# Performance work log

Measured on AMD Instinct MI355X. Metric: run time of the kernel, lower is better.

## Reference

```python
import jax, jax.numpy as jnp
import numpy as np
import math

B, S, D = 2, 2048, 1024
H, KV, HD = 16, 4, 64
G = H // KV          # kv groups
CAP = 50.0           # attention soft-cap
EPS = 1e-6           # RMSNorm eps


def _rmsnorm(x, w):
    return x * jax.lax.rsqrt(jnp.mean(x * x, axis=-1, keepdims=True) + EPS) * w


def _rope(x, freqs):
    # x: (b, h, s, hd); freqs: (S, hd//2, 2) with [...,0]=cos, [...,1]=sin
    s = x.shape[2]
    xp = x.reshape(*x.shape[:-1], -1, 2)
    cos = freqs[:s, :, 0][None, None]   # (1,1,s,hd//2)
    sin = freqs[:s, :, 1][None, None]
    x0, x1 = xp[..., 0], xp[..., 1]
    out = jnp.stack([x0 * cos - x1 * sin, x0 * sin + x1 * cos], axis=-1)
    return out.reshape(x.shape)


def setup_inputs() -> dict:
    key = jax.random.key(0)
    ks = jax.random.split(key, 6)
    x = jax.random.normal(ks[0], (B, S, D), dtype=jnp.float32)
    # realistic RoPE table: theta_i = pos / 10000^(2i/hd)
    inv_freq = 1.0 / (10000.0 ** (np.arange(0, HD, 2, dtype=np.float32) / HD))
    theta = np.arange(S, dtype=np.float32)[:, None] * inv_freq[None, :]
    rope_freqs = jnp.asarray(np.stack([np.cos(theta), np.sin(theta)], axis=-1))
    sc = 0.02
    wq = jax.random.normal(ks[1], (2 * H * HD, D), dtype=jnp.float32) * sc
    wk = jax.random.normal(ks[2], (2 * KV * HD, D), dtype=jnp.float32) * sc
    wv = jax.random.normal(ks[3], (KV * HD, D), dtype=jnp.float32) * sc
    wo = jax.random.normal(ks[4], (D, H * HD), dtype=jnp.float32) * sc
    q_norm_w = jnp.ones((HD,), dtype=jnp.float32)
    k_norm_w = jnp.ones((HD,), dtype=jnp.float32)
    diff_lambda = jnp.array([0.8], dtype=jnp.float32)
    return {"x": x, "rope_freqs": rope_freqs, "wq": wq, "wk": wk, "wv": wv,
            "wo": wo, "q_norm_w": q_norm_w, "k_norm_w": k_norm_w,
            "diff_lambda": diff_lambda}


def reference(x, rope_freqs, wq, wk, wv, wo, q_norm_w, k_norm_w, diff_lambda):
    b, s, _ = x.shape
    # projections (torch Linear: y = x @ W^T)
    q = (x @ wq.T).reshape(b, s, H, 2 * HD).transpose(0, 2, 1, 3)   # (b,H,s,2hd)
    k = (x @ wk.T).reshape(b, s, KV, 2 * HD).transpose(0, 2, 1, 3)  # (b,KV,s,2hd)
    v = (x @ wv.T).reshape(b, s, KV, HD).transpose(0, 2, 1, 3)      # (b,KV,s,hd)
    q1, q2 = jnp.split(q, 2, axis=-1)
    k1, k2 = jnp.split(k, 2, axis=-1)
    # QK-norm (before RoPE, as in the torch module)
    q1, q2 = _rmsnorm(q1, q_norm_w), _rmsnorm(q2, q_norm_w)
    k1, k2 = _rmsnorm(k1, k_norm_w), _rmsnorm(k2, k_norm_w)
    # RoPE
    q1, q2 = _rope(q1, rope_freqs), _rope(q2, rope_freqs)
    k1, k2 = _rope(k1, rope_freqs), _rope(k2, rope_freqs)
    # GQA expansion: each kv head repeated G times contiguously
    k1 = jnp.repeat(k1, G, axis=1)
    k2 = jnp.repeat(k2, G, axis=1)
    v = jnp.repeat(v, G, axis=1)
    scale = 1.0 / math.sqrt(HD)
    scores1 = jnp.einsum('bhqd,bhkd->bhqk', q1, k1) * scale
    scores2 = jnp.einsum('bhqd,bhkd->bhqk', q2, k2) * scale
    # soft-cap
    scores1 = CAP * jnp.tanh(scores1 / CAP)
    scores2 = CAP * jnp.tanh(scores2 / CAP)
    mask = jnp.triu(jnp.full((s, s), -jnp.inf, dtype=scores1.dtype), 1)
    attn1 = jax.nn.softmax(scores1 + mask, axis=-1)
    attn2 = jax.nn.softmax(scores2 + mask, axis=-1)
    diff_attn = attn1 - diff_lambda[0] * attn2
    out = jnp.einsum('bhqk,bhkd->bhqd', diff_attn, v)
    out = out.transpose(0, 2, 1, 3).reshape(b, s, H * HD)
    return out @ wo.T
```

## Files before the change

kernel.cpp:

```cpp
#include <hip/hip_runtime.h>
#include <hip/hip_bf16.h>

#define B_ 2
#define S_ 2048
#define D_ 1024
#define H_ 16
#define KV_ 4
#define HD_ 64
#define G_ (H_ / KV_)
#define NCAT 2816
#define VOFF 2560

typedef __attribute__((ext_vector_type(8))) short short8;
typedef __attribute__((ext_vector_type(4))) short short4v;
typedef __attribute__((ext_vector_type(2))) int int2v;
typedef __attribute__((ext_vector_type(4))) int int4v;
typedef __attribute__((ext_vector_type(4))) float floatx4;

using gvoid_p = const __attribute__((address_space(1))) void*;
using lvoid_p = __attribute__((address_space(3))) void*;

__device__ inline void gload_lds16(const short* g, short* l) {
    __builtin_amdgcn_global_load_lds((gvoid_p)(const void*)g, (lvoid_p)(void*)l, 16, 0, 0);
}

__device__ inline int cvt_pk_bf16(float lo, float hi) {
    int r;
    asm volatile("v_cvt_pk_bf16_f32 %0, %1, %2" : "=v"(r) : "v"(lo), "v"(hi));
    return r;
}

__global__ void cvt5_kernel(const float* s0, const float* s1, const float* s2,
                            const float* s3, const float* s4,
                            __hip_bfloat16* d0, __hip_bfloat16* d1, __hip_bfloat16* d2,
                            __hip_bfloat16* d3, __hip_bfloat16* d4,
                            int n0, int n1, int n2, int n3, int n4) {
    const float* s; __hip_bfloat16* d; int n;
    switch (blockIdx.y) {
        case 0: s = s0; d = d0; n = n0; break;
        case 1: s = s1; d = d1; n = n1; break;
        case 2: s = s2; d = d2; n = n2; break;
        case 3: s = s3; d = d3; n = n3; break;
        default: s = s4; d = d4; n = n4; break;
    }
    int nv = n >> 2;
    for (int i = blockIdx.x * blockDim.x + threadIdx.x; i < nv;
         i += gridDim.x * blockDim.x) {
        floatx4 v = ((const floatx4*)s)[i];
        short4v o;
#pragma unroll
        for (int e = 0; e < 4; ++e) {
            __hip_bfloat16 hh = __float2bfloat16(v[e]);
            o[e] = __builtin_bit_cast(short, hh);
        }
        ((short4v*)d)[i] = o;
    }
}

template <typename OutT>
__global__ __launch_bounds__(256) void gemm_bt_lds(const short* __restrict__ A,
                                                   const short* __restrict__ Bm,
                                                   OutT* __restrict__ C,
                                                   int M, int N, int K) {
    __shared__ __align__(16) short As[2][128 * 32];
    __shared__ __align__(16) short Bs[2][128 * 32];
    int tid = threadIdx.x;
    int wid = tid >> 6, lane = tid & 63;
    int wr = wid >> 1, wc = wid & 1;
    int r = lane & 15, kq = lane >> 4;

    int nwg = gridDim.x * gridDim.y;
    int orig = blockIdx.y * gridDim.x + blockIdx.x;
    int wg = (orig & 7) * (nwg >> 3) + (orig >> 3);
    int bx = wg % gridDim.x, by = wg / gridDim.x;

    long m0 = (long)by * 128;
    long n0 = (long)bx * 128;

    const short* gA0 = A + (m0 + (tid >> 2)) * (long)K + (tid & 3) * 8;
    const short* gA1 = A + (m0 + 64 + (tid >> 2)) * (long)K + (tid & 3) * 8;
    const short* gB0 = Bm + (n0 + (tid >> 2)) * (long)K + (tid & 3) * 8;
    const short* gB1 = Bm + (n0 + 64 + (tid >> 2)) * (long)K + (tid & 3) * 8;

    auto stage = [&](int buf, int k0) {
        gload_lds16(gA0 + k0, &As[buf][wid * 512]);
        gload_lds16(gA1 + k0, &As[buf][2048 + wid * 512]);
        gload_lds16(gB0 + k0, &Bs[buf][wid * 512]);
        gload_lds16(gB1 + k0, &Bs[buf][2048 + wid * 512]);
    };

    floatx4 acc[4][4];
#pragma unroll
    for (int i = 0; i < 4; ++i)
#pragma unroll
        for (int j = 0; j < 4; ++j) acc[i][j] = {0.f, 0.f, 0.f, 0.f};

    int nt = K >> 5;
    stage(0, 0);
    for (int t = 0; t < nt; ++t) {
        int cur = t & 1;
        __builtin_amdgcn_s_barrier();
        if (t + 1 < nt) {
            stage(cur ^ 1, (t + 1) << 5);
            asm volatile("s_waitcnt vmcnt(4)" ::: "memory");
        } else {
            asm volatile("s_waitcnt vmcnt(0)" ::: "memory");
        }
        __builtin_amdgcn_sched_barrier(0);
        __builtin_amdgcn_s_barrier();
        short8 a[4], b[4];
#pragma unroll
        for (int mi = 0; mi < 4; ++mi)
            a[mi] = *(const short8*)&As[cur][(wr * 64 + mi * 16 + r) * 32 + kq * 8];
#pragma unroll
        for (int ni = 0; ni < 4; ++ni)
            b[ni] = *(const short8*)&Bs[cur][(wc * 64 + ni * 16 + r) * 32 + kq * 8];
#pragma unroll
        for (int mi = 0; mi < 4; ++mi)
#pragma unroll
            for (int ni = 0; ni < 4; ++ni)
                acc[mi][ni] = __builtin_amdgcn_mfma_f32_16x16x32_bf16(
                    a[mi], b[ni], acc[mi][ni], 0, 0, 0);
    }
    int col_l = lane & 15, row_l = (lane >> 4) * 4;
#pragma unroll
    for (int mi = 0; mi < 4; ++mi)
#pragma unroll
        for (int ni = 0; ni < 4; ++ni) {
            long col = n0 + wc * 64 + ni * 16 + col_l;
            long row0 = m0 + wr * 64 + mi * 16 + row_l;
#pragma unroll
            for (int j = 0; j < 4; ++j) {
                float v = acc[mi][ni][j];
                if constexpr (__is_same(OutT, float))
                    C[(row0 + j) * N + col] = v;
                else
                    C[(row0 + j) * N + col] = __float2bfloat16(v);
            }
        }
}

__global__ void norm_rope_kernel(const __hip_bfloat16* __restrict__ buf,
                                 __hip_bfloat16* __restrict__ outb,
                                 const float* __restrict__ freqs,
                                 const float* __restrict__ w, int nvec, int nh,
                                 int tstride, int colbase) {
    int gt = blockIdx.x * blockDim.x + threadIdx.x;
    int gw = gt >> 6;
    int lane = gt & 63;
    if (gw >= nvec) return;
    int t = gw / (nh * 2);
    int rem = gw - t * (nh * 2);
    int s = t & (S_ - 1);
    const __hip_bfloat16* v = buf + (long)t * tstride + colbase + rem * 64;
    float x = __bfloat162float(v[lane]);
    float ss = x * x;
#pragma unroll
    for (int off = 32; off; off >>= 1) ss += __shfl_xor(ss, off);
    float r = rsqrtf(ss * (1.f / 64.f) + 1e-6f);
    x = x * r * w[lane];
    int i = lane >> 1;
    float c  = freqs[(s * (HD_ / 2) + i) * 2];
    float sn = freqs[(s * (HD_ / 2) + i) * 2 + 1];
    float p = __shfl_xor(x, 1);
    float y = (lane & 1) ? fmaf(p, sn, x * c) : fmaf(x, c, -(p * sn));
    outb[(long)gw * 64 + lane] = __float2bfloat16(y);
}

__global__ __launch_bounds__(256) void v_transpose_kernel(const short* __restrict__ src,
                                                          short* __restrict__ dst) {
    __shared__ short ls[64][72];
    int s0 = blockIdx.x * 64;
    int kv = blockIdx.y, b = blockIdx.z;
    int tid = threadIdx.x;
    const short* base = src + ((long)(b * S_ + s0)) * NCAT + VOFF + kv * 64;
    {
        int rr = tid >> 2, cc = (tid & 3) * 16;
        *(short8*)&ls[rr][cc]     = *(const short8*)(base + (long)rr * NCAT + cc);
        *(short8*)&ls[rr][cc + 8] = *(const short8*)(base + (long)rr * NCAT + cc + 8);
    }
    __syncthreads();
    short* ob = dst + ((long)(b * KV_ + kv) * 64) * S_ + s0;
    {
        int d = tid >> 2, sl = (tid & 3) * 16;
        short8 o0, o1;
#pragma unroll
        for (int e = 0; e < 8; ++e) { o0[e] = ls[sl + e][d]; o1[e] = ls[sl + 8 + e][d]; }
        *(short8*)(ob + (long)d * S_ + sl)     = o0;
        *(short8*)(ob + (long)d * S_ + sl + 8) = o1;
    }
}

__global__ __launch_bounds__(256, 4) void attn_kernel(const short* __restrict__ qb,
                                                      const short* __restrict__ kbuf,
                                                      const short* __restrict__ vtb,
                                                      __hip_bfloat16* __restrict__ ob,
                                                      float* __restrict__ part,
                                                      float* __restrict__ lpart,
                                                      const float* __restrict__ lam_p) {
    __shared__ __align__(16) short Ks[3][32][128];
    __shared__ __align__(16) short Vt[2][64][40];

    int tid = threadIdx.x, w = tid >> 6, lane = tid & 63;
    int b = blockIdx.z, h = blockIdx.y, kv = h / G_;
    int p = (int)blockIdx.x >> 1, e = (int)blockIdx.x & 1;
    int qtA = p, qtB = 31 - p;
    int r = lane & 15, kq = lane >> 4;
    float lam = lam_p[0];

    floatx4 acc[2][4];
    floatx4 accl[2];
    short8 qa[2][2];

    const short* vbase = vtb + (long)(b * KV_ + kv) * 64 * S_;
    const float c1 = 0.18033688f, nc4 = -3.7570e-7f, zoff = -17.3123405f;
    const short one_bf = (short)0x3F80;
    short8 ones8 = {one_bf, one_bf, one_bf, one_bf, one_bf, one_bf, one_bf, one_bf};

    int ch1 = tid + 256;
    int krow0 = tid >> 4, kcs0 = ((tid & 15) ^ (krow0 & 7)) * 8;
    int krow1 = ch1 >> 4, kcs1 = ((ch1 & 15) ^ (krow1 & 7)) * 8;
    const short* kgb = kbuf + ((long)b * S_ * KV_ + kv) * 128;
    int vd = tid >> 2, vch = tid & 3;

    auto issueK = [&](int buf, int ki) {
        long rb = (long)(ki * 32) * (KV_ * 128);
        gload_lds16(kgb + rb + (long)krow0 * (KV_ * 128) + kcs0, &Ks[buf][0][0] + w * 512);
        gload_lds16(kgb + rb + (long)krow1 * (KV_ * 128) + kcs1, &Ks[buf][0][0] + 2048 + w * 512);
    };
    auto loadV = [&](int kb) {
        return *(const short8*)(vbase + (long)vd * S_ + kb + vch * 8);
    };

    auto reset_acc = [&]() {
#pragma unroll
        for (int m = 0; m < 2; ++m) {
            accl[m] = {0.f, 0.f, 0.f, 0.f};
#pragma unroll
            for (int dt = 0; dt < 4; ++dt) acc[m][dt] = {0.f, 0.f, 0.f, 0.f};
        }
    };
    auto load_q = [&](int q0) {
        const short* qrow = qb + ((long)(b * S_ + q0 + r) * H_ + h) * 128;
        qa[0][0] = *(const short8*)(qrow + kq * 8);
        qa[0][1] = *(const short8*)(qrow + 32 + kq * 8);
        qa[1][0] = *(const short8*)(qrow + 64 + kq * 8);
        qa[1][1] = *(const short8*)(qrow + 96 + kq * 8);
    };

    auto tile_compute = [&](int bk, int cv, int kb, int q0, bool domask) {
        int rel = q0 + r - kb;
        short8 vb[4];
#pragma unroll
        for (int dt = 0; dt < 4; ++dt) {
            const short* vrow = &Vt[cv][dt * 16 + r][0];
            int2v lo = *(const int2v*)(vrow + 4 * kq);
            int2v hi = *(const int2v*)(vrow + 16 + 4 * kq);
            vb[dt] = __builtin_bit_cast(short8, int4v{lo[0], lo[1], hi[0], hi[1]});
        }
#pragma unroll
        for (int m = 0; m < 2; ++m) {
            floatx4 sacc[2];
#pragma unroll
            for (int nt = 0; nt < 2; ++nt) {
                sacc[nt] = {0.f, 0.f, 0.f, 0.f};
                const short* row = &Ks[bk][nt * 16 + r][0];
                short8 a0 = *(const short8*)(row + (((m * 8) + kq) ^ (r & 7)) * 8);
                short8 a1 = *(const short8*)(row + (((m * 8) + 4 + kq) ^ (r & 7)) * 8);
                sacc[nt] = __builtin_amdgcn_mfma_f32_16x16x32_bf16(a0, qa[m][0], sacc[nt], 0, 0, 0);
                sacc[nt] = __builtin_amdgcn_mfma_f32_16x16x32_bf16(a1, qa[m][1], sacc[nt], 0, 0, 0);
            }
            float pv[2][4];
#pragma unroll
            for (int nt = 0; nt < 2; ++nt)
#pragma unroll
                for (int j = 0; j < 4; ++j) {
                    float raw = sacc[nt][j];
                    float r2 = raw * raw;
                    float z = fmaf(raw, fmaf(r2, nc4, c1), zoff);
                    pv[nt][j] = __builtin_amdgcn_exp2f(z);
                }
            if (domask) {
#pragma unroll
                for (int nt = 0; nt < 2; ++nt)
#pragma unroll
                    for (int j = 0; j < 4; ++j)
                        if (nt * 16 + kq * 4 + j > rel) pv[nt][j] = 0.f;
            }
            int d0 = cvt_pk_bf16(pv[0][0], pv[0][1]);
            int d1 = cvt_pk_bf16(pv[0][2], pv[0][3]);
            int d2 = cvt_pk_bf16(pv[1][0], pv[1][1]);
            int d3 = cvt_pk_bf16(pv[1][2], pv[1][3]);
            short8 pa8 = __builtin_bit_cast(short8, int4v{d0, d1, d2, d3});
#pragma unroll
            for (int dt = 0; dt < 4; ++dt)
                acc[m][dt] = __builtin_amdgcn_mfma_f32_16x16x32_bf16(
                    pa8, vb[dt], acc[m][dt], 0, 0, 0);
            accl[m] = __builtin_amdgcn_mfma_f32_16x16x32_bf16(pa8, ones8, accl[m], 0, 0, 0);
        }
    };

    auto run = [&](int qt, int ki0, int ki1, bool diag) {
        int q0 = qt * 64 + w * 16;
        load_q(q0);
        reset_acc();
        int nseg = ki1 - ki0;
        issueK(0, ki0);
        short8 rva = loadV(ki0 * 32), rvb;
        int bk = 0;
        for (int ii = 0; ii < nseg; ++ii) {
            int ki = ki0 + ii, cv = ii & 1;
            bool pre = (ii + 1 < nseg);
            int bk1 = (bk == 2) ? 0 : bk + 1;
            if (pre) issueK(bk1, ki + 1);
            if (pre) asm volatile("s_waitcnt vmcnt(2)" ::: "memory");
            else     asm volatile("s_waitcnt vmcnt(0)" ::: "memory");
            __builtin_amdgcn_sched_barrier(0);
            if (cv == 0) {
                *(short8*)&Vt[0][vd][vch * 8] = rva;
                if (pre) rvb = loadV((ki + 1) * 32);
            } else {
                *(short8*)&Vt[1][vd][vch * 8] = rvb;
                if (pre) rva = loadV((ki + 1) * 32);
            }
            asm volatile("s_waitcnt lgkmcnt(0)" ::: "memory");
            __builtin_amdgcn_sched_barrier(0);
            __builtin_amdgcn_s_barrier();
            tile_compute(bk, cv, ki * 32, q0, diag && ((ki >> 1) == qt));
            bk = bk1;
        }
        __builtin_amdgcn_s_barrier();
    };

    if (e == 0) {
        run(qtA, 0, 2 * qtA + 2, true);
        {
            int q0 = qtA * 64 + w * 16;
#pragma unroll
            for (int j = 0; j < 4; ++j) {
                float i1 = 1.f / accl[0][j];
                float i2 = lam / accl[1][j];
                int qr = q0 + kq * 4 + j;
                __hip_bfloat16* orow = ob + ((long)(b * S_ + qr) * H_ + h) * 64;
#pragma unroll
                for (int dt = 0; dt < 4; ++dt) {
                    float val = acc[0][dt][j] * i1 - acc[1][dt][j] * i2;
                    orow[dt * 16 + r] = __float2bfloat16(val);
                }
            }
        }
        run(qtB, 0, 31 - 2 * p, false);
    } else {
        run(qtB, 31 - 2 * p, 64 - 2 * p, true);
    }

    {
        long slot = (long)(b * H_ + h) * 16 + (qtB - 16);
        long base = ((slot * 2 + e) * 2) * 4096L;
        int qloc = w * 16 + kq * 4;
#pragma unroll
        for (int m = 0; m < 2; ++m)
#pragma unroll
            for (int dt = 0; dt < 4; ++dt)
#pragma unroll
                for (int j = 0; j < 4; ++j)
                    part[base + m * 4096L + (qloc + j) * 64 + dt * 16 + r] = acc[m][dt][j];
        if (r == 0) {
#pragma unroll
            for (int m = 0; m < 2; ++m)
#pragma unroll
                for (int j = 0; j < 4; ++j)
                    lpart[((slot * 2 + e) * 2 + m) * 64 + qloc + j] = accl[m][j];
        }
    }
}

__global__ __launch_bounds__(256) void attn_merge_kernel(const float* __restrict__ part,
                                                         const float* __restrict__ lpart,
                                                         __hip_bfloat16* __restrict__ ob,
                                                         const float* __restrict__ lam_p) {
    long sid = blockIdx.x;
    int t16 = sid & 15;
    int h = (sid >> 4) & (H_ - 1);
    int b = (int)(sid >> 8);
    int qt = 16 + t16;
    float lam = lam_p[0];
    const float* p0 = part + sid * 4 * 4096L;
    const float* p1 = part + (sid * 4 + 2) * 4096L;
    const float* l0 = lpart + sid * 4 * 64L;
    const float* l1 = lpart + (sid * 4 + 2) * 64L;
    int tid = threadIdx.x;
#pragma unroll
    for (int i = 0; i < 16; ++i) {
        int idx = i * 256 + tid;
        int q = idx >> 6, d = idx & 63;
        float a1 = p0[q * 64 + d] + p1[q * 64 + d];
        float a2 = p0[4096 + q * 64 + d] + p1[4096 + q * 64 + d];
        float L1 = l0[q] + l1[q];
        float L2 = l0[64 + q] + l1[64 + q];
        float val = a1 / L1 - lam * (a2 / L2);
        ob[((long)(b * S_ + qt * 64 + q) * H_ + h) * 64 + d] = __float2bfloat16(val);
    }
}

extern "C" void kernel_launch(void* const* d_in, const int* in_sizes, int n_in,
                              void* d_out, int out_size, void* d_ws, size_t ws_size,
                              hipStream_t stream) {
    const float* x     = (const float*)d_in[0];
    const float* freqs = (const float*)d_in[1];
    const float* wq    = (const float*)d_in[2];
    const float* wk    = (const float*)d_in[3];
    const float* wv    = (const float*)d_in[4];
    const float* wo    = (const float*)d_in[5];
    const float* qnw   = (const float*)d_in[6];
    const float* knw   = (const float*)d_in[7];
    const float* lam   = (const float*)d_in[8];
    float* out = (float*)d_out;

    const int T = B_ * S_;
    char* ws = (char*)d_ws;
    size_t off = 0;
    auto alloc = [&](size_t bytes) {
        void* p = ws + off;
        off += (bytes + 255) & ~(size_t)255;
        return p;
    };
    __hip_bfloat16* xb   = (__hip_bfloat16*)alloc((size_t)T * D_ * 2);
    __hip_bfloat16* wcat = (__hip_bfloat16*)alloc((size_t)NCAT * D_ * 2);
    __hip_bfloat16* wob  = (__hip_bfloat16*)alloc((size_t)D_ * D_ * 2);
    __hip_bfloat16* qkvb = (__hip_bfloat16*)alloc((size_t)T * NCAT * 2);
    __hip_bfloat16* qb16 = (__hip_bfloat16*)alloc((size_t)T * 2 * H_ * HD_ * 2);
    __hip_bfloat16* kb16 = (__hip_bfloat16*)alloc((size_t)T * 2 * KV_ * HD_ * 2);
    __hip_bfloat16* vT   = (__hip_bfloat16*)alloc((size_t)B_ * KV_ * HD_ * S_ * 2);
    float* part  = (float*)alloc((size_t)512 * 2 * 2 * 4096 * 4);
    float* lpart = (float*)alloc((size_t)512 * 2 * 2 * 64 * 4);
    __hip_bfloat16* aob  = xb;

    cvt5_kernel<<<dim3(2048, 5), 256, 0, stream>>>(
        x, wq, wk, wv, wo,
        xb, wcat, wcat + (size_t)2 * H_ * HD_ * D_,
        wcat + (size_t)(2 * H_ * HD_ + 2 * KV_ * HD_) * D_, wob,
        T * D_, 2 * H_ * HD_ * D_, 2 * KV_ * HD_ * D_, KV_ * HD_ * D_, D_ * D_);

    gemm_bt_lds<__hip_bfloat16><<<dim3(NCAT / 128, T / 128), 256, 0, stream>>>(
        (const short*)xb, (const short*)wcat, qkvb, T, NCAT, D_);

    {
        int nvq = T * H_ * 2;
        norm_rope_kernel<<<(nvq * 64 + 255) / 256, 256, 0, stream>>>(
            qkvb, qb16, freqs, qnw, nvq, H_, NCAT, 0);
        int nvk = T * KV_ * 2;
        norm_rope_kernel<<<(nvk * 64 + 255) / 256, 256, 0, stream>>>(
            qkvb, kb16, freqs, knw, nvk, KV_, NCAT, 2 * H_ * HD_);
        v_transpose_kernel<<<dim3(S_ / 64, KV_, B_), 256, 0, stream>>>(
            (const short*)qkvb, (short*)vT);
    }

    attn_kernel<<<dim3(32, H_, B_), 256, 0, stream>>>(
        (const short*)qb16, (const short*)kb16, (const short*)vT, aob, part, lpart, lam);
    attn_merge_kernel<<<512, 256, 0, stream>>>(part, lpart, aob, lam);

    gemm_bt_lds<float><<<dim3(D_ / 128, T / 128), 256, 0, stream>>>(
        (const short*)aob, (const short*)wob, out, T, D_, D_);
}
```

Before: 174.6 us.

## Remap attention grid per XCD, add MFMA priority hints, pack partials to bf16

```diff
diff --git a/kernel.cpp b/kernel.cpp
--- a/kernel.cpp
+++ b/kernel.cpp
@@ -28,6 +28,13 @@
     int r;
     asm volatile("v_cvt_pk_bf16_f32 %0, %1, %2" : "=v"(r) : "v"(lo), "v"(hi));
     return r;
+}
+
+__device__ inline float bf16lo(unsigned u) {
+    return __builtin_bit_cast(float, u << 16);
+}
+__device__ inline float bf16hi(unsigned u) {
+    return __builtin_bit_cast(float, u & 0xffff0000u);
 }
 
 __global__ void cvt5_kernel(const float* s0, const float* s1, const float* s2,
@@ -195,15 +202,20 @@
                                                       const short* __restrict__ kbuf,
                                                       const short* __restrict__ vtb,
                                                       __hip_bfloat16* __restrict__ ob,
-                                                      float* __restrict__ part,
+                                                      unsigned* __restrict__ part,
                                                       float* __restrict__ lpart,
                                                       const float* __restrict__ lam_p) {
     __shared__ __align__(16) short Ks[3][32][128];
     __shared__ __align__(16) short Vt[2][64][40];
 
     int tid = threadIdx.x, w = tid >> 6, lane = tid & 63;
-    int b = blockIdx.z, h = blockIdx.y, kv = h / G_;
-    int p = (int)blockIdx.x >> 1, e = (int)blockIdx.x & 1;
+    int raw = (int)blockIdx.x;
+    int xcd = raw & 7;
+    int kv = xcd & 3, b = xcd >> 2;
+    int i5 = raw >> 3;
+    int x = i5 & 31, hh = i5 >> 5;
+    int h = kv * G_ + hh;
+    int p = x >> 1, e = x & 1;
     int qtA = p, qtB = 31 - p;
     int r = lane & 15, kq = lane >> 4;
     float lam = lam_p[0];
@@ -261,6 +273,7 @@
 #pragma unroll
         for (int m = 0; m < 2; ++m) {
             floatx4 sacc[2];
+            __builtin_amdgcn_s_setprio(1);
 #pragma unroll
             for (int nt = 0; nt < 2; ++nt) {
                 sacc[nt] = {0.f, 0.f, 0.f, 0.f};
@@ -270,14 +283,15 @@
                 sacc[nt] = __builtin_amdgcn_mfma_f32_16x16x32_bf16(a0, qa[m][0], sacc[nt], 0, 0, 0);
                 sacc[nt] = __builtin_amdgcn_mfma_f32_16x16x32_bf16(a1, qa[m][1], sacc[nt], 0, 0, 0);
             }
+            __builtin_amdgcn_s_setprio(0);
             float pv[2][4];
 #pragma unroll
             for (int nt = 0; nt < 2; ++nt)
 #pragma unroll
                 for (int j = 0; j < 4; ++j) {
-                    float raw = sacc[nt][j];
-                    float r2 = raw * raw;
-                    float z = fmaf(raw, fmaf(r2, nc4, c1), zoff);
+                    float rawv = sacc[nt][j];
+                    float r2 = rawv * rawv;
+                    float z = fmaf(rawv, fmaf(r2, nc4, c1), zoff);
                     pv[nt][j] = __builtin_amdgcn_exp2f(z);
                 }
             if (domask) {
@@ -292,11 +306,13 @@
             int d2 = cvt_pk_bf16(pv[1][0], pv[1][1]);
             int d3 = cvt_pk_bf16(pv[1][2], pv[1][3]);
             short8 pa8 = __builtin_bit_cast(short8, int4v{d0, d1, d2, d3});
+            __builtin_amdgcn_s_setprio(1);
 #pragma unroll
             for (int dt = 0; dt < 4; ++dt)
                 acc[m][dt] = __builtin_amdgcn_mfma_f32_16x16x32_bf16(
                     pa8, vb[dt], acc[m][dt], 0, 0, 0);
             accl[m] = __builtin_amdgcn_mfma_f32_16x16x32_bf16(pa8, ones8, accl[m], 0, 0, 0);
+            __builtin_amdgcn_s_setprio(0);
         }
     };
 
@@ -356,15 +372,14 @@
 
     {
         long slot = (long)(b * H_ + h) * 16 + (qtB - 16);
-        long base = ((slot * 2 + e) * 2) * 4096L;
+        long base = (slot * 2 + e) * 4096L;
         int qloc = w * 16 + kq * 4;
 #pragma unroll
-        for (int m = 0; m < 2; ++m)
-#pragma unroll
-            for (int dt = 0; dt < 4; ++dt)
-#pragma unroll
-                for (int j = 0; j < 4; ++j)
-                    part[base + m * 4096L + (qloc + j) * 64 + dt * 16 + r] = acc[m][dt][j];
+        for (int dt = 0; dt < 4; ++dt)
+#pragma unroll
+            for (int j = 0; j < 4; ++j)
+                part[base + (qloc + j) * 64 + dt * 16 + r] =
+                    (unsigned)cvt_pk_bf16(acc[0][dt][j], acc[1][dt][j]);
         if (r == 0) {
 #pragma unroll
             for (int m = 0; m < 2; ++m)
@@ -375,7 +390,7 @@
     }
 }
 
-__global__ __launch_bounds__(256) void attn_merge_kernel(const float* __restrict__ part,
+__global__ __launch_bounds__(256) void attn_merge_kernel(const unsigned* __restrict__ part,
                                                          const float* __restrict__ lpart,
                                                          __hip_bfloat16* __restrict__ ob,
                                                          const float* __restrict__ lam_p) {
@@ -385,8 +400,8 @@
     int b = (int)(sid >> 8);
     int qt = 16 + t16;
     float lam = lam_p[0];
-    const float* p0 = part + sid * 4 * 4096L;
-    const float* p1 = part + (sid * 4 + 2) * 4096L;
+    const unsigned* p0 = part + sid * 2 * 4096L;
+    const unsigned* p1 = part + (sid * 2 + 1) * 4096L;
     const float* l0 = lpart + sid * 4 * 64L;
     const float* l1 = lpart + (sid * 4 + 2) * 64L;
     int tid = threadIdx.x;
@@ -394,8 +409,9 @@
     for (int i = 0; i < 16; ++i) {
         int idx = i * 256 + tid;
         int q = idx >> 6, d = idx & 63;
-        float a1 = p0[q * 64 + d] + p1[q * 64 + d];
-        float a2 = p0[4096 + q * 64 + d] + p1[4096 + q * 64 + d];
+        unsigned u0 = p0[q * 64 + d], u1 = p1[q * 64 + d];
+        float a1 = bf16lo(u0) + bf16lo(u1);
+        float a2 = bf16hi(u0) + bf16hi(u1);
         float L1 = l0[q] + l1[q];
         float L2 = l0[64 + q] + l1[64 + q];
         float val = a1 / L1 - lam * (a2 / L2);
@@ -432,8 +448,8 @@
     __hip_bfloat16* qb16 = (__hip_bfloat16*)alloc((size_t)T * 2 * H_ * HD_ * 2);
     __hip_bfloat16* kb16 = (__hip_bfloat16*)alloc((size_t)T * 2 * KV_ * HD_ * 2);
     __hip_bfloat16* vT   = (__hip_bfloat16*)alloc((size_t)B_ * KV_ * HD_ * S_ * 2);
-    float* part  = (float*)alloc((size_t)512 * 2 * 2 * 4096 * 4);
-    float* lpart = (float*)alloc((size_t)512 * 2 * 2 * 64 * 4);
+    unsigned* part = (unsigned*)alloc((size_t)512 * 2 * 4096 * 4);
+    float* lpart   = (float*)alloc((size_t)512 * 2 * 2 * 64 * 4);
     __hip_bfloat16* aob  = xb;
 
     cvt5_kernel<<<dim3(2048, 5), 256, 0, stream>>>(
@@ -456,7 +472,7 @@
             (const short*)qkvb, (short*)vT);
     }
 
-    attn_kernel<<<dim3(32, H_, B_), 256, 0, stream>>>(
+    attn_kernel<<<1024, 256, 0, stream>>>(
         (const short*)qb16, (const short*)kb16, (const short*)vT, aob, part, lpart, lam);
     attn_merge_kernel<<<512, 256, 0, stream>>>(part, lpart, aob, lam);
 
```

New measurement: 171.5 us. Within noise of the previous version (-1.8%).
